# Kernel tuning notes

Hardware: AMD Instinct MI355X
Metric: run time of the kernel (lower is better)

Reference implementation:

```python
import jax, jax.numpy as jnp
import numpy as np

B, T, NE = 8, 4096, 1024
E, TOPK = 16, 2
LIN = NE + 32 + NE // 4 + NE // 4 + NE // 8 + NE // 8  # 1824
N_CITIES = 4


def setup_inputs() -> dict:
    key = jax.random.key(0)
    ks = jax.random.split(key, 11)
    s = 1.0 / np.sqrt(LIN)
    return {
        "mh_output": jax.random.normal(ks[0], (B, T, NE), jnp.float32),
        "delta_t_info": jax.random.normal(ks[1], (B, T, NE // 4), jnp.float32),
        "delta_dis_info": jax.random.normal(ks[2], (B, T, NE // 4), jnp.float32),
        "delta_rg_info": jax.random.normal(ks[3], (B, T, NE // 8), jnp.float32),
        "delta_entropy_info": jax.random.normal(ks[4], (B, T, NE // 8), jnp.float32),
        "city_embeddings": jax.random.normal(ks[5], (N_CITIES, 32), jnp.float32),
        "w_route": jax.random.uniform(ks[6], (LIN, E), jnp.float32, -s, s),
        "b_route": jax.random.uniform(ks[7], (E,), jnp.float32, -s, s),
        "w_noise": jax.random.uniform(ks[8], (LIN, E), jnp.float32, -s, s),
        "b_noise": jax.random.uniform(ks[9], (E,), jnp.float32, -s, s),
        "noise_eps": jax.random.normal(ks[10], (B, T, E), jnp.float32),
        "city_index": 0,
    }


def reference(mh_output, delta_t_info, delta_dis_info, delta_rg_info,
              delta_entropy_info, city_embeddings, w_route, b_route,
              w_noise, b_noise, noise_eps, city_index):
    b, t, _ = mh_output.shape
    city_embed = city_embeddings[city_index]  # [32]
    city_embeds = jnp.broadcast_to(city_embed[None, None, :], (b, t, 32))
    x = jnp.concatenate([mh_output, city_embeds, delta_t_info, delta_dis_info,
                         delta_rg_info, delta_entropy_info], axis=-1)  # [B,T,LIN]
    logits = jnp.einsum('btf,fe->bte', x, w_route) + b_route
    noise_logits = jnp.einsum('btf,fe->bte', x, w_noise) + b_noise
    noisy_logits = logits + noise_eps * jax.nn.softplus(noise_logits)  # training path
    gate1 = jax.nn.softmax(noisy_logits, axis=-1)
    top_k_logits, indices = jax.lax.top_k(noisy_logits, TOPK)  # [B,T,K]
    # scatter top-k values into a -inf tensor == mask non-topk entries to -inf
    mask = jnp.sum(jax.nn.one_hot(indices, noisy_logits.shape[-1], dtype=jnp.bool_), axis=-2) > 0
    sparse_logits = jnp.where(mask, noisy_logits, -jnp.inf)
    router_output = jax.nn.softmax(sparse_logits, axis=-1)
    return router_output, indices, gate1
```

## Files before the change

kernel.cpp:

```cpp
#include <hip/hip_runtime.h>
#include <math.h>


#define TOK_PER_BLOCK 64
#define CHUNKS_PER_WAVE 7
#define I_OFF 524288
#define G_OFF 589824

__device__ __forceinline__ float softplus_f(float x) {
  return fmaxf(x, 0.0f) + log1pf(expf(-fabsf(x)));
}

__device__ __forceinline__ float get_comp(const float4& v, int kk) {
  return kk == 0 ? v.x : kk == 1 ? v.y : kk == 2 ? v.z : v.w;
}

#define DO_FMA(AV, J)                               \
  {                                                 \
    float s_ = (AV);                                \
    accL[J].x = fmaf(s_, wl.x, accL[J].x);          \
    accL[J].y = fmaf(s_, wl.y, accL[J].y);          \
    accL[J].z = fmaf(s_, wl.z, accL[J].z);          \
    accL[J].w = fmaf(s_, wl.w, accL[J].w);          \
    accH[J].x = fmaf(s_, wh.x, accH[J].x);          \
    accH[J].y = fmaf(s_, wh.y, accH[J].y);          \
    accH[J].z = fmaf(s_, wh.z, accH[J].z);          \
    accH[J].w = fmaf(s_, wh.w, accH[J].w);          \
  }

__global__ __launch_bounds__(256, 2) void router_kernel(
    const float* __restrict__ mh, const float* __restrict__ dt,
    const float* __restrict__ dd, const float* __restrict__ rg,
    const float* __restrict__ de, const float* __restrict__ cemb_all,
    const float* __restrict__ w_route, const float* __restrict__ b_route,
    const float* __restrict__ w_noise, const float* __restrict__ b_noise,
    const float* __restrict__ eps, const int* __restrict__ city_index,
    float* __restrict__ out) {
  __shared__ float smem[8448];
  __shared__ float city_l[32];

  const int tid = threadIdx.x;
  const int w   = tid >> 6;
  const int ln  = tid & 63;
  const int tg  = ln & 15;
  const int eg  = ln >> 4;
  const int blockTok = blockIdx.x * TOK_PER_BLOCK;

  if (tid < 32) {
    const int e = tid & 15;
    const float* wsrc = (tid < 16) ? w_route : w_noise;
    const float* bsrc = (tid < 16) ? b_route : b_noise;
    const float* ce = cemb_all + city_index[0] * 32;
    float s = bsrc[e];
#pragma unroll
    for (int j = 0; j < 32; ++j) s = fmaf(ce[j], wsrc[(1024 + j) * 16 + e], s);
    city_l[tid] = s;
  }

  float4 accL[4], accH[4];
#pragma unroll
  for (int j = 0; j < 4; ++j) {
    accL[j] = make_float4(0.f, 0.f, 0.f, 0.f);
    accH[j] = make_float4(0.f, 0.f, 0.f, 0.f);
  }

  const int gbase = w * CHUNKS_PER_WAVE;
  float4 wreg[8];

  auto load_wchunk = [&](int g, float4* r) {
    const int krow_base = g * 64 + ((g * 64 >= 1024) ? 32 : 0);
#pragma unroll
    for (int rr = 0; rr < 8; ++rr) {
      int idx = rr * 64 + ln;
      int row = idx >> 3, c4 = idx & 7;
      const float* src = (c4 < 4)
          ? (w_route + (krow_base + row) * 16 + c4 * 4)
          : (w_noise + (krow_base + row) * 16 + (c4 - 4) * 4);
      r[rr] = *(const float4*)src;
    }
  };

  load_wchunk(gbase, wreg);

  float* WL = &smem[w * 2048];
  const float* WLr = WL + eg * 8;

  for (int c = 0; c < CHUNKS_PER_WAVE; ++c) {
    const int g = gbase + c;

    __syncthreads();
#pragma unroll
    for (int rr = 0; rr < 8; ++rr) {
      int idx = rr * 64 + ln;
      int row = idx >> 3, c4 = idx & 7;
      *(float4*)&WL[row * 32 + c4 * 4] = wreg[rr];
    }
    __syncthreads();

    if (c + 1 < CHUNKS_PER_WAVE) load_wchunk(g + 1, wreg);

    const float* base; int stride;
    if (g < 16)      { base = mh + g * 64;        stride = 1024; }
    else if (g < 20) { base = dt + (g - 16) * 64; stride = 256; }
    else if (g < 24) { base = dd + (g - 20) * 64; stride = 256; }
    else if (g < 26) { base = rg + (g - 24) * 64; stride = 128; }
    else             { base = de + (g - 26) * 64; stride = 128; }

    const int t0 = blockTok + tg * 4;
    const float* A0 = base + (size_t)(t0 + 0) * stride;
    const float* A1 = base + (size_t)(t0 + 1) * stride;
    const float* A2 = base + (size_t)(t0 + 2) * stride;
    const float* A3 = base + (size_t)(t0 + 3) * stride;

#pragma unroll 4
    for (int q = 0; q < 16; ++q) {
      float4 a0 = *(const float4*)(A0 + q * 4);
      float4 a1 = *(const float4*)(A1 + q * 4);
      float4 a2 = *(const float4*)(A2 + q * 4);
      float4 a3 = *(const float4*)(A3 + q * 4);
#pragma unroll
      for (int kk = 0; kk < 4; ++kk) {
        const int k = q * 4 + kk;
        float4 wl = *(const float4*)(WLr + k * 32);
        float4 wh = *(const float4*)(WLr + k * 32 + 4);
        DO_FMA(get_comp(a0, kk), 0);
        DO_FMA(get_comp(a1, kk), 1);
        DO_FMA(get_comp(a2, kk), 2);
        DO_FMA(get_comp(a3, kk), 3);
      }
    }
  }

  __syncthreads();
#pragma unroll
  for (int j = 0; j < 4; ++j) {
    float* srow = &smem[(tg * 4 + j) * 132 + w * 32 + eg * 8];
    *(float4*)(srow)     = accL[j];
    *(float4*)(srow + 4) = accH[j];
  }
  __syncthreads();

  if (tid < 64) {
    const int tokg = blockTok + tid;
    float l[32];
#pragma unroll
    for (int e4 = 0; e4 < 8; ++e4) {
      float4 s0 = *(const float4*)&smem[tid * 132 + 0 * 32 + e4 * 4];
      float4 s1 = *(const float4*)&smem[tid * 132 + 1 * 32 + e4 * 4];
      float4 s2 = *(const float4*)&smem[tid * 132 + 2 * 32 + e4 * 4];
      float4 s3 = *(const float4*)&smem[tid * 132 + 3 * 32 + e4 * 4];
      l[e4 * 4 + 0] = s0.x + s1.x + s2.x + s3.x + city_l[e4 * 4 + 0];
      l[e4 * 4 + 1] = s0.y + s1.y + s2.y + s3.y + city_l[e4 * 4 + 1];
      l[e4 * 4 + 2] = s0.z + s1.z + s2.z + s3.z + city_l[e4 * 4 + 2];
      l[e4 * 4 + 3] = s0.w + s1.w + s2.w + s3.w + city_l[e4 * 4 + 3];
    }

    const float* ep = eps + (size_t)tokg * 16;
    float n[16];
#pragma unroll
    for (int e = 0; e < 16; ++e)
      n[e] = fmaf(ep[e], softplus_f(l[16 + e]), l[e]);

    float m1 = -INFINITY; int i1 = 0;
#pragma unroll
    for (int e = 0; e < 16; ++e)
      if (n[e] > m1) { m1 = n[e]; i1 = e; }
    float m2 = -INFINITY; int i2 = 0;
#pragma unroll
    for (int e = 0; e < 16; ++e)
      if (e != i1 && n[e] > m2) { m2 = n[e]; i2 = e; }

    float ex[16], Z = 0.f;
#pragma unroll
    for (int e = 0; e < 16; ++e) { ex[e] = expf(n[e] - m1); Z += ex[e]; }
    const float invZ  = 1.0f / Z;
    const float invZ2 = 1.0f / (1.0f + expf(m2 - m1));

    float r[16], g1[16];
#pragma unroll
    for (int e = 0; e < 16; ++e) {
      r[e]  = (e == i1 || e == i2) ? ex[e] * invZ2 : 0.0f;
      g1[e] = ex[e] * invZ;
    }

    float* ro = out + (size_t)tokg * 16;
#pragma unroll
    for (int e4 = 0; e4 < 4; ++e4)
      *(float4*)(ro + e4 * 4) = make_float4(r[e4 * 4], r[e4 * 4 + 1], r[e4 * 4 + 2], r[e4 * 4 + 3]);

    out[I_OFF + (size_t)tokg * 2 + 0] = (float)i1;
    out[I_OFF + (size_t)tokg * 2 + 1] = (float)i2;

    float* go = out + G_OFF + (size_t)tokg * 16;
#pragma unroll
    for (int e4 = 0; e4 < 4; ++e4)
      *(float4*)(go + e4 * 4) = make_float4(g1[e4 * 4], g1[e4 * 4 + 1], g1[e4 * 4 + 2], g1[e4 * 4 + 3]);
  }
}

extern "C" void kernel_launch(void* const* d_in, const int* in_sizes, int n_in,
                              void* d_out, int out_size, void* d_ws, size_t ws_size,
                              hipStream_t stream) {
  const float* mh = (const float*)d_in[0];
  const float* dt = (const float*)d_in[1];
  const float* dd = (const float*)d_in[2];
  const float* rg = (const float*)d_in[3];
  const float* de = (const float*)d_in[4];
  const float* ce = (const float*)d_in[5];
  const float* wr = (const float*)d_in[6];
  const float* br = (const float*)d_in[7];
  const float* wn = (const float*)d_in[8];
  const float* bn = (const float*)d_in[9];
  const float* ep = (const float*)d_in[10];
  const int*   ci = (const int*)d_in[11];
  float* out = (float*)d_out;

  router_kernel<<<512, 256, 0, stream>>>(mh, dt, dd, rg, de, ce, wr, br, wn, bn,
                                         ep, ci, out);
}
```

Measured before the change: 367.0 us.

## Stage activation tiles through LDS with coalesced loads and smaller token blocks

Each block now handles 32 tokens and walks all 28 K-chunks. Every chunk's activation tile and weight tile are loaded cooperatively with coalesced float4 loads into padded shared memory, with a register prefetch of the next chunk. Before, each wave read strided activation rows straight from global memory. Waves now split K within a chunk instead of splitting chunks, and the grid doubles with launch bounds raised to 4 blocks per CU. The cost is two barriers per chunk and more LDS traffic per FMA.

```diff
diff --git a/kernel.cpp b/kernel.cpp
--- a/kernel.cpp
+++ b/kernel.cpp
@@ -2,11 +2,15 @@
 #include <math.h>
 
 
-#define TOK_PER_BLOCK 64
-#define CHUNKS_PER_WAVE 7
+#define TOKS 32
+#define NCHUNK 28
 #define I_OFF 524288
 #define G_OFF 589824
 
+#define SA_STRIDE 68
+#define SW_STRIDE 36
+#define SS_STRIDE 132
+
 __device__ __forceinline__ float softplus_f(float x) {
   return fmaxf(x, 0.0f) + log1pf(expf(-fabsf(x)));
 }
@@ -15,20 +19,7 @@
   return kk == 0 ? v.x : kk == 1 ? v.y : kk == 2 ? v.z : v.w;
 }
 
-#define DO_FMA(AV, J)                               \
-  {                                                 \
-    float s_ = (AV);                                \
-    accL[J].x = fmaf(s_, wl.x, accL[J].x);          \
-    accL[J].y = fmaf(s_, wl.y, accL[J].y);          \
-    accL[J].z = fmaf(s_, wl.z, accL[J].z);          \
-    accL[J].w = fmaf(s_, wl.w, accL[J].w);          \
-    accH[J].x = fmaf(s_, wh.x, accH[J].x);          \
-    accH[J].y = fmaf(s_, wh.y, accH[J].y);          \
-    accH[J].z = fmaf(s_, wh.z, accH[J].z);          \
-    accH[J].w = fmaf(s_, wh.w, accH[J].w);          \
-  }
-
-__global__ __launch_bounds__(256, 2) void router_kernel(
+__global__ __launch_bounds__(256, 4) void router_kernel(
     const float* __restrict__ mh, const float* __restrict__ dt,
     const float* __restrict__ dd, const float* __restrict__ rg,
     const float* __restrict__ de, const float* __restrict__ cemb_all,
@@ -36,15 +27,23 @@
     const float* __restrict__ w_noise, const float* __restrict__ b_noise,
     const float* __restrict__ eps, const int* __restrict__ city_index,
     float* __restrict__ out) {
-  __shared__ float smem[8448];
+  __shared__ float smem[4480];
   __shared__ float city_l[32];
+  float* sA = smem;
+  float* sW = smem + 2176;
+  float* sS = smem;
 
   const int tid = threadIdx.x;
   const int w   = tid >> 6;
   const int ln  = tid & 63;
-  const int tg  = ln & 15;
-  const int eg  = ln >> 4;
-  const int blockTok = blockIdx.x * TOK_PER_BLOCK;
+  const int tg  = ln & 7;
+  const int eg  = ln >> 3;
+  const int blockTok = blockIdx.x * TOKS;
+
+  const int ar0 = tid >> 4,        ac0 = (tid & 15) * 4;
+  const int ar1 = (tid + 256) >> 4, ac1 = (tid & 15) * 4;
+  const int wr0 = tid >> 3,        wc0 = tid & 7;
+  const int wr1 = (tid + 256) >> 3, wc1 = tid & 7;
 
   if (tid < 32) {
     const int e = tid & 15;
@@ -57,98 +56,94 @@
     city_l[tid] = s;
   }
 
-  float4 accL[4], accH[4];
-#pragma unroll
-  for (int j = 0; j < 4; ++j) {
-    accL[j] = make_float4(0.f, 0.f, 0.f, 0.f);
-    accH[j] = make_float4(0.f, 0.f, 0.f, 0.f);
-  }
-
-  const int gbase = w * CHUNKS_PER_WAVE;
-  float4 wreg[8];
-
-  auto load_wchunk = [&](int g, float4* r) {
-    const int krow_base = g * 64 + ((g * 64 >= 1024) ? 32 : 0);
-#pragma unroll
-    for (int rr = 0; rr < 8; ++rr) {
-      int idx = rr * 64 + ln;
-      int row = idx >> 3, c4 = idx & 7;
-      const float* src = (c4 < 4)
-          ? (w_route + (krow_base + row) * 16 + c4 * 4)
-          : (w_noise + (krow_base + row) * 16 + (c4 - 4) * 4);
-      r[rr] = *(const float4*)src;
-    }
-  };
-
-  load_wchunk(gbase, wreg);
-
-  float* WL = &smem[w * 2048];
-  const float* WLr = WL + eg * 8;
-
-  for (int c = 0; c < CHUNKS_PER_WAVE; ++c) {
-    const int g = gbase + c;
-
-    __syncthreads();
-#pragma unroll
-    for (int rr = 0; rr < 8; ++rr) {
-      int idx = rr * 64 + ln;
-      int row = idx >> 3, c4 = idx & 7;
-      *(float4*)&WL[row * 32 + c4 * 4] = wreg[rr];
-    }
-    __syncthreads();
-
-    if (c + 1 < CHUNKS_PER_WAVE) load_wchunk(g + 1, wreg);
-
+  float4 acc0 = make_float4(0.f,0.f,0.f,0.f);
+  float4 acc1 = make_float4(0.f,0.f,0.f,0.f);
+  float4 acc2 = make_float4(0.f,0.f,0.f,0.f);
+  float4 acc3 = make_float4(0.f,0.f,0.f,0.f);
+
+  float4 Areg0, Areg1, Wreg0, Wreg1;
+
+  auto a_src = [&](int g, int row) -> const float* {
     const float* base; int stride;
     if (g < 16)      { base = mh + g * 64;        stride = 1024; }
     else if (g < 20) { base = dt + (g - 16) * 64; stride = 256; }
     else if (g < 24) { base = dd + (g - 20) * 64; stride = 256; }
     else if (g < 26) { base = rg + (g - 24) * 64; stride = 128; }
     else             { base = de + (g - 26) * 64; stride = 128; }
-
-    const int t0 = blockTok + tg * 4;
-    const float* A0 = base + (size_t)(t0 + 0) * stride;
-    const float* A1 = base + (size_t)(t0 + 1) * stride;
-    const float* A2 = base + (size_t)(t0 + 2) * stride;
-    const float* A3 = base + (size_t)(t0 + 3) * stride;
-
-#pragma unroll 4
-    for (int q = 0; q < 16; ++q) {
-      float4 a0 = *(const float4*)(A0 + q * 4);
-      float4 a1 = *(const float4*)(A1 + q * 4);
-      float4 a2 = *(const float4*)(A2 + q * 4);
-      float4 a3 = *(const float4*)(A3 + q * 4);
+    return base + (size_t)(blockTok + row) * stride;
+  };
+
+  auto prefetch = [&](int g) {
+    Areg0 = *(const float4*)(a_src(g, ar0) + ac0);
+    Areg1 = *(const float4*)(a_src(g, ar1) + ac1);
+    const int kb = g * 64 + ((g * 64 >= 1024) ? 32 : 0);
+    const float* s0 = (wc0 < 4) ? (w_route + (kb + wr0) * 16 + wc0 * 4)
+                                : (w_noise + (kb + wr0) * 16 + (wc0 - 4) * 4);
+    const float* s1 = (wc1 < 4) ? (w_route + (kb + wr1) * 16 + wc1 * 4)
+                                : (w_noise + (kb + wr1) * 16 + (wc1 - 4) * 4);
+    Wreg0 = *(const float4*)s0;
+    Wreg1 = *(const float4*)s1;
+  };
+
+  prefetch(0);
+
+  for (int c = 0; c < NCHUNK; ++c) {
+    __syncthreads();
+    *(float4*)&sA[ar0 * SA_STRIDE + ac0] = Areg0;
+    *(float4*)&sA[ar1 * SA_STRIDE + ac1] = Areg1;
+    *(float4*)&sW[wr0 * SW_STRIDE + wc0 * 4] = Wreg0;
+    *(float4*)&sW[wr1 * SW_STRIDE + wc1 * 4] = Wreg1;
+    __syncthreads();
+
+    if (c + 1 < NCHUNK) prefetch(c + 1);
+
+#pragma unroll
+    for (int qq = 0; qq < 4; ++qq) {
+      const int koff = w * 16 + qq * 4;
+      float4 a0 = *(const float4*)&sA[(tg +  0) * SA_STRIDE + koff];
+      float4 a1 = *(const float4*)&sA[(tg +  8) * SA_STRIDE + koff];
+      float4 a2 = *(const float4*)&sA[(tg + 16) * SA_STRIDE + koff];
+      float4 a3 = *(const float4*)&sA[(tg + 24) * SA_STRIDE + koff];
 #pragma unroll
       for (int kk = 0; kk < 4; ++kk) {
-        const int k = q * 4 + kk;
-        float4 wl = *(const float4*)(WLr + k * 32);
-        float4 wh = *(const float4*)(WLr + k * 32 + 4);
-        DO_FMA(get_comp(a0, kk), 0);
-        DO_FMA(get_comp(a1, kk), 1);
-        DO_FMA(get_comp(a2, kk), 2);
-        DO_FMA(get_comp(a3, kk), 3);
+        float4 wv = *(const float4*)&sW[(koff + kk) * SW_STRIDE + eg * 4];
+        float s;
+        s = get_comp(a0, kk);
+        acc0.x = fmaf(s, wv.x, acc0.x); acc0.y = fmaf(s, wv.y, acc0.y);
+        acc0.z = fmaf(s, wv.z, acc0.z); acc0.w = fmaf(s, wv.w, acc0.w);
+        s = get_comp(a1, kk);
+        acc1.x = fmaf(s, wv.x, acc1.x); acc1.y = fmaf(s, wv.y, acc1.y);
+        acc1.z = fmaf(s, wv.z, acc1.z); acc1.w = fmaf(s, wv.w, acc1.w);
+        s = get_comp(a2, kk);
+        acc2.x = fmaf(s, wv.x, acc2.x); acc2.y = fmaf(s, wv.y, acc2.y);
+        acc2.z = fmaf(s, wv.z, acc2.z); acc2.w = fmaf(s, wv.w, acc2.w);
+        s = get_comp(a3, kk);
+        acc3.x = fmaf(s, wv.x, acc3.x); acc3.y = fmaf(s, wv.y, acc3.y);
+        acc3.z = fmaf(s, wv.z, acc3.z); acc3.w = fmaf(s, wv.w, acc3.w);
       }
     }
   }
 
   __syncthreads();
-#pragma unroll
-  for (int j = 0; j < 4; ++j) {
-    float* srow = &smem[(tg * 4 + j) * 132 + w * 32 + eg * 8];
-    *(float4*)(srow)     = accL[j];
-    *(float4*)(srow + 4) = accH[j];
+  {
+    float* s0 = &sS[(tg +  0) * SS_STRIDE + w * 32 + eg * 4];
+    float* s1 = &sS[(tg +  8) * SS_STRIDE + w * 32 + eg * 4];
+    float* s2 = &sS[(tg + 16) * SS_STRIDE + w * 32 + eg * 4];
+    float* s3 = &sS[(tg + 24) * SS_STRIDE + w * 32 + eg * 4];
+    *(float4*)s0 = acc0; *(float4*)s1 = acc1;
+    *(float4*)s2 = acc2; *(float4*)s3 = acc3;
   }
   __syncthreads();
 
-  if (tid < 64) {
+  if (tid < TOKS) {
     const int tokg = blockTok + tid;
     float l[32];
 #pragma unroll
     for (int e4 = 0; e4 < 8; ++e4) {
-      float4 s0 = *(const float4*)&smem[tid * 132 + 0 * 32 + e4 * 4];
-      float4 s1 = *(const float4*)&smem[tid * 132 + 1 * 32 + e4 * 4];
-      float4 s2 = *(const float4*)&smem[tid * 132 + 2 * 32 + e4 * 4];
-      float4 s3 = *(const float4*)&smem[tid * 132 + 3 * 32 + e4 * 4];
+      float4 s0 = *(const float4*)&sS[tid * SS_STRIDE +  0 + e4 * 4];
+      float4 s1 = *(const float4*)&sS[tid * SS_STRIDE + 32 + e4 * 4];
+      float4 s2 = *(const float4*)&sS[tid * SS_STRIDE + 64 + e4 * 4];
+      float4 s3 = *(const float4*)&sS[tid * SS_STRIDE + 96 + e4 * 4];
       l[e4 * 4 + 0] = s0.x + s1.x + s2.x + s3.x + city_l[e4 * 4 + 0];
       l[e4 * 4 + 1] = s0.y + s1.y + s2.y + s3.y + city_l[e4 * 4 + 1];
       l[e4 * 4 + 2] = s0.z + s1.z + s2.z + s3.z + city_l[e4 * 4 + 2];
@@ -186,7 +181,7 @@
     float* ro = out + (size_t)tokg * 16;
 #pragma unroll
     for (int e4 = 0; e4 < 4; ++e4)
-      *(float4*)(ro + e4 * 4) = make_float4(r[e4 * 4], r[e4 * 4 + 1], r[e4 * 4 + 2], r[e4 * 4 + 3]);
+      *(float4*)(ro + e4 * 4) = make_float4(r[e4*4], r[e4*4+1], r[e4*4+2], r[e4*4+3]);
 
     out[I_OFF + (size_t)tokg * 2 + 0] = (float)i1;
     out[I_OFF + (size_t)tokg * 2 + 1] = (float)i2;
@@ -194,7 +189,7 @@
     float* go = out + G_OFF + (size_t)tokg * 16;
 #pragma unroll
     for (int e4 = 0; e4 < 4; ++e4)
-      *(float4*)(go + e4 * 4) = make_float4(g1[e4 * 4], g1[e4 * 4 + 1], g1[e4 * 4 + 2], g1[e4 * 4 + 3]);
+      *(float4*)(go + e4 * 4) = make_float4(g1[e4*4], g1[e4*4+1], g1[e4*4+2], g1[e4*4+3]);
   }
 }
 
@@ -215,6 +210,6 @@
   const int*   ci = (const int*)d_in[11];
   float* out = (float*)d_out;
 
-  router_kernel<<<512, 256, 0, stream>>>(mh, dt, dd, rg, de, ce, wr, br, wn, bn,
-                                         ep, ci, out);
-}
+  router_kernel<<<1024, 256, 0, stream>>>(mh, dt, dd, rg, de, ce, wr, br, wn, bn,
+                                          ep, ci, out);
+}
```

Result: faster. 304.2 us (-17.1%).
